# Optimization experiments

Measured on AMD Instinct MI355X. Metric: run time of the kernel, lower is better.

Reference implementation:

```python
import jax, jax.numpy as jnp
import numpy as np

N = 100000  # nodes
E = 600000  # edges (avg degree ~6, mesh-like)
HID = 128


def _lin(key, fan_in, fan_out):
    # torch Linear default init: U(-1/sqrt(fan_in), 1/sqrt(fan_in))
    bound = 1.0 / np.sqrt(fan_in)
    return jax.random.uniform(key, (fan_in, fan_out), jnp.float32, -bound, bound)


def setup_inputs() -> dict:
    key = jax.random.key(0)
    ks = jax.random.split(key, 8)
    x = jax.random.normal(ks[0], (N, 3), jnp.float32)
    edge_index = jax.random.randint(ks[1], (2, E), 0, N, dtype=jnp.int32)
    return {
        "x": x,
        "edge_index": edge_index,
        "W1": _lin(ks[2], 3, HID),          "b1": jnp.zeros((HID,), jnp.float32),
        "W2": _lin(ks[3], HID, HID),        "b2": jnp.zeros((HID,), jnp.float32),
        "W3": _lin(ks[4], HID, HID // 2),   "b3": jnp.zeros((HID // 2,), jnp.float32),
        "W4": _lin(ks[5], HID // 2, HID // 2), "b4": jnp.zeros((HID // 2,), jnp.float32),
        "W5": _lin(ks[6], HID // 2, 1),     "b5": jnp.zeros((1,), jnp.float32),
    }


def reference(x, edge_index, W1, b1, W2, b2, W3, b3, W4, b4, W5, b5):
    n = x.shape[0]
    # add self loops (same graph used by every layer)
    loops = jnp.arange(n, dtype=edge_index.dtype)
    row = jnp.concatenate([edge_index[0], loops])  # sources (x_j index)
    col = jnp.concatenate([edge_index[1], loops])  # targets (aggregation index)
    # symmetric degree normalization: norm_e = d[row]^-0.5 * d[col]^-0.5
    deg = jax.ops.segment_sum(jnp.ones(col.shape, x.dtype), col, num_segments=n)
    dis = jnp.where(deg > 0, deg ** -0.5, 0.0)
    norm = (dis[row] * dis[col])[:, None]  # [E+N, 1]

    def conv(h, W, b):
        h = h @ W                                   # [N, out]
        msg = norm * h[row]                         # gather + scale  [E+N, out]
        return jax.ops.segment_sum(msg, col, num_segments=n) + b  # scatter-add

    h = jax.nn.relu(conv(x, W1, b1))
    h = jax.nn.relu(conv(h, W2, b2))
    h = jax.nn.relu(conv(h, W3, b3))
    h = jax.nn.relu(conv(h, W4, b4))
    return conv(h, W5, b5)  # [N, 1]
```

## Files before the change

### kernel.cpp

```cpp
#include <hip/hip_runtime.h>
#include <hip/hip_bf16.h>
#include <stdint.h>


#define NB 256
#define CAP 64

typedef __attribute__((ext_vector_type(8))) short bf16x8;
typedef __attribute__((ext_vector_type(4))) float f32x4;

static __host__ __device__ inline int ceil_div(int a, int b) { return (a + b - 1) / b; }

__device__ inline ushort f32_to_bf16(float x) {
    uint32_t u = __float_as_uint(x);
    uint32_t r = (u + 0x7fffu + ((u >> 16) & 1u)) >> 16;
    return (ushort)r;
}
__device__ inline float bf16_lo(uint32_t u) { return __uint_as_float(u << 16); }
__device__ inline float bf16_hi(uint32_t u) { return __uint_as_float(u & 0xffff0000u); }


template <int K, int F>
__device__ inline void pack_one(const float* __restrict__ W, ushort* __restrict__ Wp, int id) {
    constexpr int KS = K / 32;
    int j = id & 7;
    int lane = (id >> 3) & 63;
    int ts = id >> 9;
    int s = ts % KS;
    int t = ts / KS;
    int k = s * 32 + ((lane >> 4) << 3) + j;
    int f = t * 16 + (lane & 15);
    Wp[id] = f32_to_bf16(W[k * F + f]);
}

__global__ void k_init(int* __restrict__ cursor, int n, int zero_blocks,
                       const float* __restrict__ W2, const float* __restrict__ W3,
                       const float* __restrict__ W4, ushort* __restrict__ Wp2,
                       ushort* __restrict__ Wp3, ushort* __restrict__ Wp4) {
    int b = blockIdx.x;
    if (b < zero_blocks) {
        int i = b * NB + threadIdx.x;
        if (i < n) cursor[i] = 0;
    } else {
        int id = (b - zero_blocks) * NB + threadIdx.x;
        if (id < 16384) pack_one<128, 128>(W2, Wp2, id);
        else if (id < 24576) pack_one<128, 64>(W3, Wp3, id - 16384);
        else if (id < 28672) pack_one<64, 64>(W4, Wp4, id - 24576);
    }
}


__global__ void k_fillb(const int* __restrict__ row, const int* __restrict__ col, int e,
                        int* __restrict__ cursor, int* __restrict__ bucket) {
    int T = (e + 3) >> 2;
    int t = blockIdx.x * NB + threadIdx.x;
    int i0 = t, i1 = t + T, i2 = t + 2 * T, i3 = t + 3 * T;
    if (i3 < e) {
        int c0 = col[i0], c1 = col[i1], c2 = col[i2], c3 = col[i3];
        int r0 = row[i0], r1 = row[i1], r2 = row[i2], r3 = row[i3];
        int s0 = atomicAdd(&cursor[c0], 1);
        int s1 = atomicAdd(&cursor[c1], 1);
        int s2 = atomicAdd(&cursor[c2], 1);
        int s3 = atomicAdd(&cursor[c3], 1);
        bucket[(size_t)c0 * CAP + s0] = r0;
        bucket[(size_t)c1 * CAP + s1] = r1;
        bucket[(size_t)c2 * CAP + s2] = r2;
        bucket[(size_t)c3 * CAP + s3] = r3;
    } else {
        int idx[4] = {i0, i1, i2, i3};
#pragma unroll
        for (int k = 0; k < 4; ++k) {
            int i = idx[k];
            if (i < e) {
                int c = col[i], r = row[i];
                int s = atomicAdd(&cursor[c], 1);
                bucket[(size_t)c * CAP + s] = r;
            }
        }
    }
}

__global__ void k_dis(const int* __restrict__ cnt, const float* __restrict__ x,
                      float* __restrict__ dis, float4* __restrict__ xs4, int n) {
    int i = blockIdx.x * NB + threadIdx.x;
    if (i >= n) return;
    float d = rsqrtf((float)(cnt[i] + 1));
    dis[i] = d;
    xs4[i] = make_float4(d * x[3 * i], d * x[3 * i + 1], d * x[3 * i + 2], 0.f);
}


__global__ __launch_bounds__(256) void k_l1f(const float4* __restrict__ xs4,
                                             const int* __restrict__ cnt,
                                             const int* __restrict__ bucket,
                                             const float* __restrict__ dis,
                                             const float* __restrict__ W1,
                                             const float* __restrict__ b1,
                                             ushort* __restrict__ A, int n) {
    __shared__ float w[512];
    for (int t = threadIdx.x; t < 512; t += 256)
        w[t] = (t < 384) ? W1[t] : b1[t - 384];
    __syncthreads();
    int i = blockIdx.x * NB + threadIdx.x;
    if (i >= n) return;
    float4 self = xs4[i];
    float a0 = self.x, a1 = self.y, a2 = self.z;
    int deg = cnt[i];
    const int* bk = bucket + (size_t)i * CAP;
    int e = 0;
    for (; e + 4 <= deg; e += 4) {
        int4 j4 = *(const int4*)(bk + e);
        float4 v0 = xs4[j4.x], v1 = xs4[j4.y], v2 = xs4[j4.z], v3 = xs4[j4.w];
        a0 += v0.x + v1.x + v2.x + v3.x;
        a1 += v0.y + v1.y + v2.y + v3.y;
        a2 += v0.z + v1.z + v2.z + v3.z;
    }
    for (; e < deg; ++e) {
        float4 v = xs4[bk[e]];
        a0 += v.x; a1 += v.y; a2 += v.z;
    }
    float d = dis[i];
    a0 *= d; a1 *= d; a2 *= d;
    uint4* arow = (uint4*)A + (size_t)i * 16;
#pragma unroll
    for (int f8 = 0; f8 < 16; ++f8) {
        uint32_t ov[4];
#pragma unroll
        for (int q = 0; q < 4; ++q) {
            int f = f8 * 8 + 2 * q;
            float v0 = fmaxf(a0 * w[f] + a1 * w[128 + f] + a2 * w[256 + f] + w[384 + f], 0.f);
            float v1 = fmaxf(a0 * w[f + 1] + a1 * w[128 + f + 1] + a2 * w[256 + f + 1] + w[384 + f + 1], 0.f);
            ov[q] = ((uint32_t)f32_to_bf16(v1) << 16) | (uint32_t)f32_to_bf16(v0);
        }
        arow[f8] = make_uint4(ov[0], ov[1], ov[2], ov[3]);
    }
}


template <int K, int F>
__global__ __launch_bounds__(256) void k_mmfma(const ushort* __restrict__ H,
                                               const ushort* __restrict__ Wp,
                                               const float* __restrict__ dis,
                                               ushort* __restrict__ Z, int n) {
    constexpr int KS = K / 32;
    constexpr int FT = F / 16;
    int wid = threadIdx.x >> 6;
    int lane = threadIdx.x & 63;
    int node0 = blockIdx.x * 64 + wid * 16;
    int m = lane & 15;
    int quad = lane >> 4;
    int arow = node0 + m;
    if (arow >= n) arow = n - 1;
    const bf16x8* aptr = (const bf16x8*)(H + (size_t)arow * K + quad * 8);
    bf16x8 a[KS];
#pragma unroll
    for (int s = 0; s < KS; ++s) a[s] = aptr[s * 4];
    float dsc[4];
#pragma unroll
    for (int r = 0; r < 4; ++r) {
        int node = node0 + quad * 4 + r;
        dsc[r] = (node < n) ? dis[node] : 0.f;
    }
    const bf16x8* bp = (const bf16x8*)Wp;
#pragma unroll 2
    for (int t = 0; t < FT; ++t) {
        f32x4 acc = {0.f, 0.f, 0.f, 0.f};
#pragma unroll
        for (int s = 0; s < KS; ++s)
            acc = __builtin_amdgcn_mfma_f32_16x16x32_bf16(a[s], bp[(t * KS + s) * 64 + lane], acc, 0, 0, 0);
        int feat = t * 16 + m;
#pragma unroll
        for (int r = 0; r < 4; ++r) {
            int node = node0 + quad * 4 + r;
            if (node < n) Z[(size_t)node * F + feat] = f32_to_bf16(acc[r] * dsc[r]);
        }
    }
}


__device__ inline void add8(float (&a)[8], uint4 v) {
    a[0] += bf16_lo(v.x);
    a[1] += bf16_hi(v.x);
    a[2] += bf16_lo(v.y);
    a[3] += bf16_hi(v.y);
    a[4] += bf16_lo(v.z);
    a[5] += bf16_hi(v.z);
    a[6] += bf16_lo(v.w);
    a[7] += bf16_hi(v.w);
}

template <int L>
__device__ inline void agg_sum(float (&a)[8], const uint4* __restrict__ Zq,
                               const int* __restrict__ bk, int deg, int l, int i) {
    add8(a, Zq[(size_t)i * L + l]);
    int e = 0;
    for (; e + 4 <= deg; e += 4) {
        int4 j4 = *(const int4*)(bk + e);
        uint4 v0 = Zq[(size_t)j4.x * L + l];
        uint4 v1 = Zq[(size_t)j4.y * L + l];
        uint4 v2 = Zq[(size_t)j4.z * L + l];
        uint4 v3 = Zq[(size_t)j4.w * L + l];
        add8(a, v0);
        add8(a, v1);
        add8(a, v2);
        add8(a, v3);
    }
    for (; e < deg; ++e) add8(a, Zq[(size_t)bk[e] * L + l]);
}

__device__ inline uint4 pack8s(const float (&a)[8], float d, const float* __restrict__ bias, int l) {
    float4 b0 = *(const float4*)&bias[8 * l];
    float4 b1 = *(const float4*)&bias[8 * l + 4];
    float r0 = fmaxf(a[0] * d + b0.x, 0.f), r1 = fmaxf(a[1] * d + b0.y, 0.f);
    float r2 = fmaxf(a[2] * d + b0.z, 0.f), r3 = fmaxf(a[3] * d + b0.w, 0.f);
    float r4 = fmaxf(a[4] * d + b1.x, 0.f), r5 = fmaxf(a[5] * d + b1.y, 0.f);
    float r6 = fmaxf(a[6] * d + b1.z, 0.f), r7 = fmaxf(a[7] * d + b1.w, 0.f);
    uint4 o;
    o.x = ((uint32_t)f32_to_bf16(r1) << 16) | (uint32_t)f32_to_bf16(r0);
    o.y = ((uint32_t)f32_to_bf16(r3) << 16) | (uint32_t)f32_to_bf16(r2);
    o.z = ((uint32_t)f32_to_bf16(r5) << 16) | (uint32_t)f32_to_bf16(r4);
    o.w = ((uint32_t)f32_to_bf16(r7) << 16) | (uint32_t)f32_to_bf16(r6);
    return o;
}


template <int FIN, int FOUT>
__global__ __launch_bounds__(256) void k_aggmm(const ushort* __restrict__ Zin,
                                               const float* __restrict__ bias,
                                               const int* __restrict__ cnt,
                                               const int* __restrict__ bucket,
                                               const float* __restrict__ dis,
                                               const ushort* __restrict__ Wp,
                                               ushort* __restrict__ Zout, int n) {
    constexpr int L = FIN / 8;
    constexpr int GROUPS = 256 / L;
    constexpr int PASSES = 64 / GROUPS;
    __shared__ ushort tileA[64][FIN + 8];
    int node0 = blockIdx.x * 64;

    {
        int l = threadIdx.x & (L - 1);
        int g = threadIdx.x / L;
#pragma unroll
        for (int pass = 0; pass < PASSES; ++pass) {
            int local = pass * GROUPS + g;
            int i = node0 + local;
            if (i < n) {
                float a[8] = {0.f, 0.f, 0.f, 0.f, 0.f, 0.f, 0.f, 0.f};
                agg_sum<L>(a, (const uint4*)Zin, bucket + (size_t)i * CAP, cnt[i], l, i);
                *(uint4*)&tileA[local][l * 8] = pack8s(a, dis[i], bias, l);
            }
        }
    }
    __syncthreads();

    constexpr int KS = FIN / 32;
    constexpr int FT = FOUT / 16;
    int wid = threadIdx.x >> 6;
    int lane = threadIdx.x & 63;
    int m = lane & 15;
    int quad = lane >> 4;
    int tbase = wid * 16;
    bf16x8 a[KS];
#pragma unroll
    for (int s = 0; s < KS; ++s)
        a[s] = *(const bf16x8*)&tileA[tbase + m][s * 32 + quad * 8];
    float dsc[4];
#pragma unroll
    for (int r = 0; r < 4; ++r) {
        int node = node0 + tbase + quad * 4 + r;
        dsc[r] = (node < n) ? dis[node] : 0.f;
    }
    const bf16x8* bp = (const bf16x8*)Wp;
#pragma unroll
    for (int t = 0; t < FT; ++t) {
        f32x4 acc = {0.f, 0.f, 0.f, 0.f};
#pragma unroll
        for (int s = 0; s < KS; ++s)
            acc = __builtin_amdgcn_mfma_f32_16x16x32_bf16(a[s], bp[(t * KS + s) * 64 + lane], acc, 0, 0, 0);
        int feat = t * 16 + m;
#pragma unroll
        for (int r = 0; r < 4; ++r) {
            int node = node0 + tbase + quad * 4 + r;
            if (node < n) Zout[(size_t)node * FOUT + feat] = f32_to_bf16(acc[r] * dsc[r]);
        }
    }
}

__global__ __launch_bounds__(256) void k_agg64z(const ushort* __restrict__ Z,
                                                const float* __restrict__ bias,
                                                const float* __restrict__ W5,
                                                const int* __restrict__ cnt,
                                                const int* __restrict__ bucket,
                                                const float* __restrict__ dis,
                                                float* __restrict__ zbuf, int n) {
    int l = threadIdx.x & 7;
    int i = blockIdx.x * 32 + (threadIdx.x >> 3);
    if (i >= n) return;
    float a[8] = {0.f, 0.f, 0.f, 0.f, 0.f, 0.f, 0.f, 0.f};
    agg_sum<8>(a, (const uint4*)Z, bucket + (size_t)i * CAP, cnt[i], l, i);
    float d = dis[i];
    float4 b0 = *(const float4*)&bias[8 * l];
    float4 b1 = *(const float4*)&bias[8 * l + 4];
    float4 w0 = *(const float4*)&W5[8 * l];
    float4 w1 = *(const float4*)&W5[8 * l + 4];
    float p = fmaxf(a[0] * d + b0.x, 0.f) * w0.x + fmaxf(a[1] * d + b0.y, 0.f) * w0.y +
              fmaxf(a[2] * d + b0.z, 0.f) * w0.z + fmaxf(a[3] * d + b0.w, 0.f) * w0.w +
              fmaxf(a[4] * d + b1.x, 0.f) * w1.x + fmaxf(a[5] * d + b1.y, 0.f) * w1.y +
              fmaxf(a[6] * d + b1.z, 0.f) * w1.z + fmaxf(a[7] * d + b1.w, 0.f) * w1.w;
#pragma unroll
    for (int off = 4; off; off >>= 1) p += __shfl_xor(p, off, 64);
    if (l == 0) zbuf[i] = d * p;
}

__global__ void k_agg1(const float* __restrict__ zbuf, const float* __restrict__ b5,
                       const int* __restrict__ cnt, const int* __restrict__ bucket,
                       const float* __restrict__ dis, float* __restrict__ out, int n) {
    int i = blockIdx.x * NB + threadIdx.x;
    if (i >= n) return;
    float acc = zbuf[i];
    int deg = cnt[i];
    const int* bk = bucket + (size_t)i * CAP;
    int e = 0;
    for (; e + 4 <= deg; e += 4) {
        int4 j4 = *(const int4*)(bk + e);
        acc += zbuf[j4.x] + zbuf[j4.y] + zbuf[j4.z] + zbuf[j4.w];
    }
    for (; e < deg; ++e) acc += zbuf[bk[e]];
    out[i] = dis[i] * acc + b5[0];
}


static inline size_t align_up(size_t x) { return (x + 255) & ~(size_t)255; }

extern "C" void kernel_launch(void* const* d_in, const int* in_sizes, int n_in,
                              void* d_out, int out_size, void* d_ws, size_t ws_size,
                              hipStream_t stream) {
    const int n = in_sizes[0] / 3;
    const int e = in_sizes[1] / 2;

    const float* x   = (const float*)d_in[0];
    const int*   ei  = (const int*)d_in[1];
    const int*   row = ei;
    const int*   col = ei + e;
    const float* W1 = (const float*)d_in[2];  const float* b1 = (const float*)d_in[3];
    const float* W2 = (const float*)d_in[4];  const float* b2 = (const float*)d_in[5];
    const float* W3 = (const float*)d_in[6];  const float* b3 = (const float*)d_in[7];
    const float* W4 = (const float*)d_in[8];  const float* b4 = (const float*)d_in[9];
    const float* W5 = (const float*)d_in[10]; const float* b5 = (const float*)d_in[11];
    float* out = (float*)d_out;

    char* base = (char*)d_ws;
    size_t off = 0;
    auto alloc = [&](size_t bytes) { char* p = base + off; off = align_up(off + bytes); return p; };
    int*    cursor = (int*)alloc((size_t)n * 4);
    float*  dis    = (float*)alloc((size_t)n * 4);
    float4* xs4    = (float4*)alloc((size_t)n * 16);
    int*    bucket = (int*)alloc((size_t)n * CAP * 4);
    ushort* A      = (ushort*)alloc((size_t)n * 128 * 2);
    ushort* B      = (ushort*)alloc((size_t)n * 128 * 2);
    float*  zbuf   = (float*)alloc((size_t)n * 4);
    ushort* Wp2    = (ushort*)alloc(128 * 128 * 2);
    ushort* Wp3    = (ushort*)alloc(128 * 64 * 2);
    ushort* Wp4    = (ushort*)alloc(64 * 64 * 2);
    (void)ws_size;

    const int gn = ceil_div(n, NB);
    const int pack_blocks = ceil_div(16384 + 8192 + 4096, NB);

    k_init<<<gn + pack_blocks, NB, 0, stream>>>(cursor, n, gn, W2, W3, W4, Wp2, Wp3, Wp4);
    k_fillb<<<ceil_div(ceil_div(e, 4), NB), NB, 0, stream>>>(row, col, e, cursor, bucket);
    k_dis<<<gn, NB, 0, stream>>>(cursor, x, dis, xs4, n);

    k_l1f<<<gn, NB, 0, stream>>>(xs4, cursor, bucket, dis, W1, b1, A, n);

    k_mmfma<128, 128><<<ceil_div(n, 64), 256, 0, stream>>>(A, Wp2, dis, B, n);

    k_aggmm<128, 64><<<ceil_div(n, 64), 256, 0, stream>>>(B, b2, cursor, bucket, dis, Wp3, A, n);

    k_aggmm<64, 64><<<ceil_div(n, 64), 256, 0, stream>>>(A, b3, cursor, bucket, dis, Wp4, B, n);

    k_agg64z<<<ceil_div(n, 32), 256, 0, stream>>>(B, b4, W5, cursor, bucket, dis, zbuf, n);

    k_agg1<<<gn, NB, 0, stream>>>(zbuf, b5, cursor, bucket, dis, out, n);
}
```

Before: 226.6 us.

## Fuse layer-1 aggregation with layer-2 MFMA matmul via shared-memory tile

```diff
diff --git a/kernel.cpp b/kernel.cpp
--- a/kernel.cpp
+++ b/kernel.cpp
@@ -52,27 +52,24 @@
 
 __global__ void k_fillb(const int* __restrict__ row, const int* __restrict__ col, int e,
                         int* __restrict__ cursor, int* __restrict__ bucket) {
-    int T = (e + 3) >> 2;
+    int T = (e + 7) >> 3;
     int t = blockIdx.x * NB + threadIdx.x;
-    int i0 = t, i1 = t + T, i2 = t + 2 * T, i3 = t + 3 * T;
-    if (i3 < e) {
-        int c0 = col[i0], c1 = col[i1], c2 = col[i2], c3 = col[i3];
-        int r0 = row[i0], r1 = row[i1], r2 = row[i2], r3 = row[i3];
-        int s0 = atomicAdd(&cursor[c0], 1);
-        int s1 = atomicAdd(&cursor[c1], 1);
-        int s2 = atomicAdd(&cursor[c2], 1);
-        int s3 = atomicAdd(&cursor[c3], 1);
-        bucket[(size_t)c0 * CAP + s0] = r0;
-        bucket[(size_t)c1 * CAP + s1] = r1;
-        bucket[(size_t)c2 * CAP + s2] = r2;
-        bucket[(size_t)c3 * CAP + s3] = r3;
+    int i[8];
+#pragma unroll
+    for (int k = 0; k < 8; ++k) i[k] = t + k * T;
+    if (i[7] < e) {
+        int c[8], r[8], s[8];
+#pragma unroll
+        for (int k = 0; k < 8; ++k) { c[k] = col[i[k]]; r[k] = row[i[k]]; }
+#pragma unroll
+        for (int k = 0; k < 8; ++k) s[k] = atomicAdd(&cursor[c[k]], 1);
+#pragma unroll
+        for (int k = 0; k < 8; ++k) bucket[(size_t)c[k] * CAP + s[k]] = r[k];
     } else {
-        int idx[4] = {i0, i1, i2, i3};
-#pragma unroll
-        for (int k = 0; k < 4; ++k) {
-            int i = idx[k];
-            if (i < e) {
-                int c = col[i], r = row[i];
+#pragma unroll
+        for (int k = 0; k < 8; ++k) {
+            if (i[k] < e) {
+                int c = col[i[k]], r = row[i[k]];
                 int s = atomicAdd(&cursor[c], 1);
                 bucket[(size_t)c * CAP + s] = r;
             }
@@ -90,79 +87,77 @@
 }
 
 
-__global__ __launch_bounds__(256) void k_l1f(const float4* __restrict__ xs4,
-                                             const int* __restrict__ cnt,
-                                             const int* __restrict__ bucket,
-                                             const float* __restrict__ dis,
-                                             const float* __restrict__ W1,
-                                             const float* __restrict__ b1,
-                                             ushort* __restrict__ A, int n) {
+__global__ __launch_bounds__(256) void k_l1mm(const float4* __restrict__ xs4,
+                                              const int* __restrict__ cnt,
+                                              const int* __restrict__ bucket,
+                                              const float* __restrict__ dis,
+                                              const float* __restrict__ W1,
+                                              const float* __restrict__ b1,
+                                              const ushort* __restrict__ Wp2,
+                                              ushort* __restrict__ Zout, int n) {
     __shared__ float w[512];
+    __shared__ float s_a[64][4];
+    __shared__ ushort tileH[64][136];
     for (int t = threadIdx.x; t < 512; t += 256)
         w[t] = (t < 384) ? W1[t] : b1[t - 384];
+
+    int node0 = blockIdx.x * 64;
+    int local = threadIdx.x >> 2;
+    int sub = threadIdx.x & 3;
+    int i = node0 + local;
+    float a0 = 0.f, a1 = 0.f, a2 = 0.f;
+    if (i < n) {
+        if (sub == 0) {
+            float4 self = xs4[i];
+            a0 = self.x; a1 = self.y; a2 = self.z;
+        }
+        int deg = cnt[i];
+        const int* bk = bucket + (size_t)i * CAP;
+        for (int e = sub; e < deg; e += 4) {
+            float4 v = xs4[bk[e]];
+            a0 += v.x; a1 += v.y; a2 += v.z;
+        }
+    }
+    a0 += __shfl_xor(a0, 1, 64); a1 += __shfl_xor(a1, 1, 64); a2 += __shfl_xor(a2, 1, 64);
+    a0 += __shfl_xor(a0, 2, 64); a1 += __shfl_xor(a1, 2, 64); a2 += __shfl_xor(a2, 2, 64);
+    if (sub == 0) {
+        float d = (i < n) ? dis[i] : 0.f;
+        s_a[local][0] = a0 * d;
+        s_a[local][1] = a1 * d;
+        s_a[local][2] = a2 * d;
+    }
     __syncthreads();
-    int i = blockIdx.x * NB + threadIdx.x;
-    if (i >= n) return;
-    float4 self = xs4[i];
-    float a0 = self.x, a1 = self.y, a2 = self.z;
-    int deg = cnt[i];
-    const int* bk = bucket + (size_t)i * CAP;
-    int e = 0;
-    for (; e + 4 <= deg; e += 4) {
-        int4 j4 = *(const int4*)(bk + e);
-        float4 v0 = xs4[j4.x], v1 = xs4[j4.y], v2 = xs4[j4.z], v3 = xs4[j4.w];
-        a0 += v0.x + v1.x + v2.x + v3.x;
-        a1 += v0.y + v1.y + v2.y + v3.y;
-        a2 += v0.z + v1.z + v2.z + v3.z;
-    }
-    for (; e < deg; ++e) {
-        float4 v = xs4[bk[e]];
-        a0 += v.x; a1 += v.y; a2 += v.z;
-    }
-    float d = dis[i];
-    a0 *= d; a1 *= d; a2 *= d;
-    uint4* arow = (uint4*)A + (size_t)i * 16;
-#pragma unroll
-    for (int f8 = 0; f8 < 16; ++f8) {
-        uint32_t ov[4];
-#pragma unroll
-        for (int q = 0; q < 4; ++q) {
-            int f = f8 * 8 + 2 * q;
-            float v0 = fmaxf(a0 * w[f] + a1 * w[128 + f] + a2 * w[256 + f] + w[384 + f], 0.f);
-            float v1 = fmaxf(a0 * w[f + 1] + a1 * w[128 + f + 1] + a2 * w[256 + f + 1] + w[384 + f + 1], 0.f);
-            ov[q] = ((uint32_t)f32_to_bf16(v1) << 16) | (uint32_t)f32_to_bf16(v0);
-        }
-        arow[f8] = make_uint4(ov[0], ov[1], ov[2], ov[3]);
-    }
-}
-
-
-template <int K, int F>
-__global__ __launch_bounds__(256) void k_mmfma(const ushort* __restrict__ H,
-                                               const ushort* __restrict__ Wp,
-                                               const float* __restrict__ dis,
-                                               ushort* __restrict__ Z, int n) {
-    constexpr int KS = K / 32;
-    constexpr int FT = F / 16;
+
+#pragma unroll
+    for (int it = 0; it < 16; ++it) {
+        int id = it * 256 + threadIdx.x;
+        int lc = id >> 6;
+        int f = (id & 63) * 2;
+        float h0 = s_a[lc][0], h1 = s_a[lc][1], h2 = s_a[lc][2];
+        float v0 = fmaxf(h0 * w[f] + h1 * w[128 + f] + h2 * w[256 + f] + w[384 + f], 0.f);
+        float v1 = fmaxf(h0 * w[f + 1] + h1 * w[128 + f + 1] + h2 * w[256 + f + 1] + w[384 + f + 1], 0.f);
+        *(uint32_t*)&tileH[lc][f] = ((uint32_t)f32_to_bf16(v1) << 16) | (uint32_t)f32_to_bf16(v0);
+    }
+    __syncthreads();
+
+    constexpr int KS = 4, FT = 8;
     int wid = threadIdx.x >> 6;
     int lane = threadIdx.x & 63;
-    int node0 = blockIdx.x * 64 + wid * 16;
     int m = lane & 15;
     int quad = lane >> 4;
-    int arow = node0 + m;
-    if (arow >= n) arow = n - 1;
-    const bf16x8* aptr = (const bf16x8*)(H + (size_t)arow * K + quad * 8);
+    int tbase = wid * 16;
     bf16x8 a[KS];
 #pragma unroll
-    for (int s = 0; s < KS; ++s) a[s] = aptr[s * 4];
+    for (int s = 0; s < KS; ++s)
+        a[s] = *(const bf16x8*)&tileH[tbase + m][s * 32 + quad * 8];
     float dsc[4];
 #pragma unroll
     for (int r = 0; r < 4; ++r) {
-        int node = node0 + quad * 4 + r;
+        int node = node0 + tbase + quad * 4 + r;
         dsc[r] = (node < n) ? dis[node] : 0.f;
     }
-    const bf16x8* bp = (const bf16x8*)Wp;
-#pragma unroll 2
+    const bf16x8* bp = (const bf16x8*)Wp2;
+#pragma unroll
     for (int t = 0; t < FT; ++t) {
         f32x4 acc = {0.f, 0.f, 0.f, 0.f};
 #pragma unroll
@@ -171,8 +166,8 @@
         int feat = t * 16 + m;
 #pragma unroll
         for (int r = 0; r < 4; ++r) {
-            int node = node0 + quad * 4 + r;
-            if (node < n) Z[(size_t)node * F + feat] = f32_to_bf16(acc[r] * dsc[r]);
+            int node = node0 + tbase + quad * 4 + r;
+            if (node < n) Zout[(size_t)node * 128 + feat] = f32_to_bf16(acc[r] * dsc[r]);
         }
     }
 }
@@ -369,12 +364,10 @@
     const int pack_blocks = ceil_div(16384 + 8192 + 4096, NB);
 
     k_init<<<gn + pack_blocks, NB, 0, stream>>>(cursor, n, gn, W2, W3, W4, Wp2, Wp3, Wp4);
-    k_fillb<<<ceil_div(ceil_div(e, 4), NB), NB, 0, stream>>>(row, col, e, cursor, bucket);
+    k_fillb<<<ceil_div(ceil_div(e, 8), NB), NB, 0, stream>>>(row, col, e, cursor, bucket);
     k_dis<<<gn, NB, 0, stream>>>(cursor, x, dis, xs4, n);
 
-    k_l1f<<<gn, NB, 0, stream>>>(xs4, cursor, bucket, dis, W1, b1, A, n);
-
-    k_mmfma<128, 128><<<ceil_div(n, 64), 256, 0, stream>>>(A, Wp2, dis, B, n);
+    k_l1mm<<<ceil_div(n, 64), 256, 0, stream>>>(xs4, cursor, bucket, dis, W1, b1, Wp2, B, n);
 
     k_aggmm<128, 64><<<ceil_div(n, 64), 256, 0, stream>>>(B, b2, cursor, bucket, dis, Wp3, A, n);
 
```

Result: faster. 215.1 us (-5.1%).
